# Performance work log

Hardware: AMD Instinct MI355X
Metric: run time of the kernel (lower is better)

## Reference

```python
import jax, jax.numpy as jnp
import numpy as np

N_HEADS = 16
N_EMBD = 1024

def setup_inputs() -> dict:
    key = jax.random.key(0)
    k1, k2, k3, k4, k5 = jax.random.split(key, 5)
    B, T, C = 4, 2048, N_EMBD
    x = jax.random.normal(k1, (B, T, C), dtype=jnp.float32)
    # Linear weights stored as [in, out] (equivalent math to torch's x @ W.T + b)
    W_attn = jax.random.normal(k2, (C, 3 * C), dtype=jnp.float32) * 0.02
    b_attn = jax.random.normal(k3, (3 * C,), dtype=jnp.float32) * 0.02
    W_proj = jax.random.normal(k4, (C, C), dtype=jnp.float32) * 0.02
    b_proj = jax.random.normal(k5, (C,), dtype=jnp.float32) * 0.02
    return {"x": x, "W_attn": W_attn, "b_attn": b_attn, "W_proj": W_proj, "b_proj": b_proj}

def reference(x, W_attn, b_attn, W_proj, b_proj):
    B, T, C = x.shape
    H = N_HEADS
    D = C // H
    scale = 1.0 / jnp.sqrt(jnp.asarray(D, dtype=x.dtype))
    # fused QKV projection
    qkv = x @ W_attn + b_attn                      # [B, T, 3C]
    q, k, v = jnp.split(qkv, 3, axis=-1)           # each [B, T, C]
    q = q.reshape(B, T, H, D)
    k = k.reshape(B, T, H, D)
    v = v.reshape(B, T, H, D)
    # non-causal SDPA
    scores = jnp.einsum('bqhd,bkhd->bhqk', q, k) * scale  # [B, H, T, T]
    attn = jax.nn.softmax(scores, axis=-1)
    y = jnp.einsum('bhqk,bkhd->bqhd', attn, v)     # [B, T, H, D]
    y = y.reshape(B, T, C)
    return y @ W_proj + b_proj
```

## Files before the change

### kernel.cpp

```cpp
#include <hip/hip_runtime.h>

typedef short s16x8 __attribute__((ext_vector_type(8)));
typedef short s16x4 __attribute__((ext_vector_type(4)));
typedef float f32x4 __attribute__((ext_vector_type(4)));
typedef float f32x16 __attribute__((ext_vector_type(16)));

__device__ __forceinline__ unsigned short f2bf(float f) {
  unsigned u = __float_as_uint(f);
  u += 0x7fffu + ((u >> 16) & 1u);
  return (unsigned short)(u >> 16);
}
__device__ __forceinline__ float bf2f(unsigned short h) {
  return __uint_as_float(((unsigned)h) << 16);
}

#define GLOAD_LDS16(g, l)                                          \
  __builtin_amdgcn_global_load_lds(                                \
      (const __attribute__((address_space(1))) void*)(g),          \
      (__attribute__((address_space(3))) void*)(l), 16, 0, 0)


__global__ __launch_bounds__(256) void cvt_x_bf16(const float* __restrict__ in,
                                                  unsigned short* __restrict__ out) {
  int i = (blockIdx.x * 256 + threadIdx.x) * 4;
  float4 v = *(const float4*)(in + i);
  ushort4 o;
  o.x = f2bf(v.x); o.y = f2bf(v.y); o.z = f2bf(v.z); o.w = f2bf(v.w);
  *(ushort4*)(out + i) = o;
}

__global__ __launch_bounds__(256) void transpose_w(const float* __restrict__ W,
                                                   unsigned short* __restrict__ Wt,
                                                   int R, int C) {
  __shared__ float tile[32][33];
  int c0 = blockIdx.x * 32, r0 = blockIdx.y * 32;
  int x = threadIdx.x, ty = threadIdx.y;
  for (int yy = ty; yy < 32; yy += 8)
    tile[yy][x] = W[(size_t)(r0 + yy) * C + c0 + x];
  __syncthreads();
  for (int yy = ty; yy < 32; yy += 8)
    Wt[(size_t)(c0 + yy) * R + r0 + x] = f2bf(tile[x][yy]);
}


template <int MODE>
__global__ __launch_bounds__(256) void gemm_bt(const unsigned short* __restrict__ A,
                                               const unsigned short* __restrict__ Bt,
                                               const float* __restrict__ bias,
                                               void* __restrict__ Cout,
                                               unsigned short* __restrict__ vtr,
                                               int M, int N, int K) {
  __shared__ __align__(16) unsigned short As[3][128 * 32];
  __shared__ __align__(16) unsigned short Bs[3][128 * 32];

  const int tid  = threadIdx.x;
  const int lane = tid & 63;
  const int w    = tid >> 6;
  const int lm   = lane & 31;
  const int l5   = lane >> 5;
  const int wm   = (w >> 1) * 64;
  const int wn   = (w & 1) * 64;
  const int m0   = blockIdx.x * 128;
  const int n0   = blockIdx.y * 128;

  f32x16 acc[2][2];
  for (int i = 0; i < 2; i++)
    for (int j = 0; j < 2; j++)
      for (int r = 0; r < 16; r++) acc[i][j][r] = 0.f;

  const int srow = tid >> 2;
  const int scb  = (((tid & 3) ^ ((srow >> 1) & 3)) * 8);
  const unsigned short* Ap = A  + (size_t)(m0 + srow) * K + scb;
  const unsigned short* Bp = Bt + (size_t)(n0 + srow) * K + scb;

#define STAGE_G(bb, kk)                                                  \
  do {                                                                   \
    GLOAD_LDS16(Ap + (kk), &As[bb][w * 512]);                            \
    GLOAD_LDS16(Ap + (size_t)64 * K + (kk), &As[bb][2048 + w * 512]);    \
    GLOAD_LDS16(Bp + (kk), &Bs[bb][w * 512]);                            \
    GLOAD_LDS16(Bp + (size_t)64 * K + (kk), &Bs[bb][2048 + w * 512]);    \
  } while (0)

  const int rx = ((lm >> 1) & 3) << 4;

  STAGE_G(0, 0);
  STAGE_G(1, 32);
  int cur = 0;
  for (int kk = 0; kk < K; kk += 32) {
    if (kk + 32 < K)
      asm volatile("s_waitcnt vmcnt(4)" ::: "memory");
    else
      asm volatile("s_waitcnt vmcnt(0)" ::: "memory");
    __builtin_amdgcn_s_barrier();
    __builtin_amdgcn_sched_barrier(0);

    if (kk + 64 < K) {
      int nb = cur + 2; if (nb >= 3) nb -= 3;
      STAGE_G(nb, kk + 64);
    }

    const char* Ab = (const char*)As[cur];
    const char* Bb = (const char*)Bs[cur];
    s16x8 af[2][2], bfr[2][2];
    for (int i = 0; i < 2; i++)
      for (int ks = 0; ks < 2; ks++)
        af[i][ks] = *(const s16x8*)(Ab + (wm + i * 32 + lm) * 64 +
                                    (((l5 * 16 + ks * 32)) ^ rx));
    for (int j = 0; j < 2; j++)
      for (int ks = 0; ks < 2; ks++)
        bfr[j][ks] = *(const s16x8*)(Bb + (wn + j * 32 + lm) * 64 +
                                     (((l5 * 16 + ks * 32)) ^ rx));
    for (int ks = 0; ks < 2; ks++)
      for (int i = 0; i < 2; i++)
        for (int j = 0; j < 2; j++)
          acc[i][j] = __builtin_amdgcn_mfma_f32_32x32x16_bf16(af[i][ks], bfr[j][ks],
                                                              acc[i][j], 0, 0, 0);
    cur += 1; if (cur >= 3) cur -= 3;
  }
#undef STAGE_G

  if (MODE == 1 && n0 >= 2048) {
    const int bidx = m0 >> 11;
    for (int j = 0; j < 2; j++) {
      int col = n0 + wn + j * 32 + lm;
      float bc = bias[col];
      size_t vrow = (size_t)((bidx << 10) + (col - 2048)) * 2048;
      for (int i = 0; i < 2; i++) {
        int tb = (m0 & 2047) + wm + i * 32 + l5 * 4;
        for (int g = 0; g < 4; g++) {
          ushort4 o;
          o.x = f2bf(acc[i][j][g * 4 + 0] + bc);
          o.y = f2bf(acc[i][j][g * 4 + 1] + bc);
          o.z = f2bf(acc[i][j][g * 4 + 2] + bc);
          o.w = f2bf(acc[i][j][g * 4 + 3] + bc);
          *(ushort4*)(vtr + vrow + tb + 8 * g) = o;
        }
      }
    }
  } else {
    for (int j = 0; j < 2; j++) {
      int col = n0 + wn + j * 32 + lm;
      float bc = bias[col];
      for (int i = 0; i < 2; i++) {
        int rowb = m0 + wm + i * 32 + l5 * 4;
        for (int r = 0; r < 16; r++) {
          int row = rowb + (r & 3) + 8 * (r >> 2);
          float v = acc[i][j][r] + bc;
          if (MODE == 1)
            ((unsigned short*)Cout)[(size_t)row * N + col] = f2bf(v);
          else
            ((float*)Cout)[(size_t)row * N + col] = v;
        }
      }
    }
  }
}


__global__ __launch_bounds__(256, 4) void attn_flash(const unsigned short* __restrict__ qkv,
                                                     const unsigned short* __restrict__ vt,
                                                     unsigned short* __restrict__ y) {
  const int T = 2048, C3 = 3072;
  const int bh = blockIdx.x & 63;
  const int qt = blockIdx.x >> 6;
  const int b  = bh >> 4;
  const int h  = bh & 15;
  const int q0 = qt * 128;

  const int tid  = threadIdx.x;
  const int lane = tid & 63;
  const int w    = tid >> 6;
  const int lr   = lane & 15;
  const int quad = lane >> 4;

  __shared__ __align__(16) unsigned short Ks[2][64][64];
  __shared__ __align__(16) unsigned short Vs[2][64][64];

  s16x8 qf[2][2];
  const float QSC = 0.18033688f;
  for (int j = 0; j < 2; j++)
    for (int c = 0; c < 2; c++) {
      const unsigned short* qp =
          qkv + (size_t)(b * T + q0 + w * 32 + j * 16 + lr) * C3 + h * 64 + c * 32 + quad * 8;
      s16x8 t = *(const s16x8*)qp;
      s16x8 o;
      for (int e = 0; e < 8; e++)
        o[e] = (short)f2bf(bf2f((unsigned short)t[e]) * QSC);
      qf[j][c] = o;
    }

  s16x8 ones;
  for (int e = 0; e < 8; e++) ones[e] = (short)0x3F80;

  f32x4 O[2][4];
  f32x4 Lacc[2];
  for (int j = 0; j < 2; j++) {
    for (int dt = 0; dt < 4; dt++) O[j][dt] = f32x4{0.f, 0.f, 0.f, 0.f};
    Lacc[j] = f32x4{0.f, 0.f, 0.f, 0.f};
  }

  const int srow = tid >> 3;
  const int scol = (((tid & 7) ^ (srow & 7)) * 8);
  const int kperm = (((srow & 12) << 1) | ((srow >> 4) << 2) | (srow & 3));

  const unsigned short* kbase = qkv + (size_t)(b * T) * C3 + 1024 + (size_t)h * 64;
  const unsigned short* vbase = vt + (size_t)(bh * 64) * 2048;
  const unsigned short* kp0 = kbase + (size_t)(kperm)      * C3 + scol;
  const unsigned short* kp1 = kbase + (size_t)(32 + kperm) * C3 + scol;
  const unsigned short* vp0 = vbase + (size_t)(srow)      * 2048 + scol;
  const unsigned short* vp1 = vbase + (size_t)(srow + 32) * 2048 + scol;

#define STAGE_KV(bb)                                                         \
  do {                                                                       \
    GLOAD_LDS16(kp0, &Ks[bb][w * 8][0]);                                     \
    GLOAD_LDS16(kp1, &Ks[bb][w * 8 + 32][0]);                                \
    GLOAD_LDS16(vp0, &Vs[bb][w * 8][0]);                                     \
    GLOAD_LDS16(vp1, &Vs[bb][w * 8 + 32][0]);                                \
    kp0 += (size_t)64 * C3; kp1 += (size_t)64 * C3;                          \
    vp0 += 64; vp1 += 64;                                                    \
  } while (0)

  const int rswz = (lr & 7) << 4;

#define COMPUTE(bb)                                                              \
  do {                                                                           \
    const char* KsB = (const char*)&Ks[bb][0][0];                                \
    const char* VsB = (const char*)&Vs[bb][0][0];                                \
    for (int ch = 0; ch < 2; ch++) {                                             \
      const char* krowA = KsB + (ch * 32 + lr) * 128;                            \
      const char* krowB = KsB + (ch * 32 + 16 + lr) * 128;                       \
      s16x8 kA0 = *(const s16x8*)(krowA + ((quad * 16) ^ rswz));                 \
      s16x8 kA1 = *(const s16x8*)(krowA + ((64 + quad * 16) ^ rswz));            \
      s16x8 kB0 = *(const s16x8*)(krowB + ((quad * 16) ^ rswz));                 \
      s16x8 kB1 = *(const s16x8*)(krowB + ((64 + quad * 16) ^ rswz));            \
      s16x8 vf[4];                                                               \
      for (int dt = 0; dt < 4; dt++)                                             \
        vf[dt] = *(const s16x8*)(VsB + (dt * 16 + lr) * 128 +                    \
                                 ((ch * 64 + quad * 16) ^ rswz));                \
      for (int j = 0; j < 2; j++) {                                              \
        f32x4 Sa = f32x4{0.f, 0.f, 0.f, 0.f};                                    \
        f32x4 Sb = f32x4{0.f, 0.f, 0.f, 0.f};                                    \
        __builtin_amdgcn_s_setprio(1);                                           \
        Sa = __builtin_amdgcn_mfma_f32_16x16x32_bf16(kA0, qf[j][0], Sa, 0, 0, 0);\
        Sa = __builtin_amdgcn_mfma_f32_16x16x32_bf16(kA1, qf[j][1], Sa, 0, 0, 0);\
        Sb = __builtin_amdgcn_mfma_f32_16x16x32_bf16(kB0, qf[j][0], Sb, 0, 0, 0);\
        Sb = __builtin_amdgcn_mfma_f32_16x16x32_bf16(kB1, qf[j][1], Sb, 0, 0, 0);\
        __builtin_amdgcn_s_setprio(0);                                           \
        float p0 = __builtin_amdgcn_exp2f(Sa[0]);                                \
        float p1 = __builtin_amdgcn_exp2f(Sa[1]);                                \
        float p2 = __builtin_amdgcn_exp2f(Sa[2]);                                \
        float p3 = __builtin_amdgcn_exp2f(Sa[3]);                                \
        float p4 = __builtin_amdgcn_exp2f(Sb[0]);                                \
        float p5 = __builtin_amdgcn_exp2f(Sb[1]);                                \
        float p6 = __builtin_amdgcn_exp2f(Sb[2]);                                \
        float p7 = __builtin_amdgcn_exp2f(Sb[3]);                                \
        union { unsigned u[4]; s16x8 v; } pk;                                    \
        asm("v_cvt_pk_bf16_f32 %0, %1, %2" : "=v"(pk.u[0]) : "v"(p0), "v"(p1));  \
        asm("v_cvt_pk_bf16_f32 %0, %1, %2" : "=v"(pk.u[1]) : "v"(p2), "v"(p3));  \
        asm("v_cvt_pk_bf16_f32 %0, %1, %2" : "=v"(pk.u[2]) : "v"(p4), "v"(p5));  \
        asm("v_cvt_pk_bf16_f32 %0, %1, %2" : "=v"(pk.u[3]) : "v"(p6), "v"(p7));  \
        __builtin_amdgcn_s_setprio(1);                                           \
        Lacc[j] = __builtin_amdgcn_mfma_f32_16x16x32_bf16(pk.v, ones, Lacc[j],   \
                                                          0, 0, 0);              \
        for (int dt = 0; dt < 4; dt++)                                           \
          O[j][dt] = __builtin_amdgcn_mfma_f32_16x16x32_bf16(pk.v, vf[dt],       \
                                                             O[j][dt], 0, 0, 0); \
        __builtin_amdgcn_s_setprio(0);                                           \
      }                                                                          \
    }                                                                            \
  } while (0)

  STAGE_KV(0);
  for (int kt2 = 0; kt2 < 16; kt2++) {
    __syncthreads();
    STAGE_KV(1);
    COMPUTE(0);
    __syncthreads();
    if (kt2 < 15) STAGE_KV(0);
    COMPUTE(1);
  }
#undef STAGE_KV
#undef COMPUTE

  for (int j = 0; j < 2; j++) {
    for (int r = 0; r < 4; r++) {
      float inv = 1.f / Lacc[j][r];
      int row = b * T + q0 + w * 32 + j * 16 + quad * 4 + r;
      for (int dt = 0; dt < 4; dt++) {
        int col = h * 64 + dt * 16 + lr;
        y[(size_t)row * 1024 + col] = f2bf(O[j][dt][r] * inv);
      }
    }
  }
}


extern "C" void kernel_launch(void* const* d_in, const int* in_sizes, int n_in,
                              void* d_out, int out_size, void* d_ws, size_t ws_size,
                              hipStream_t stream) {
  const float* x  = (const float*)d_in[0];
  const float* Wa = (const float*)d_in[1];
  const float* ba = (const float*)d_in[2];
  const float* Wp = (const float*)d_in[3];
  const float* bp = (const float*)d_in[4];
  float* out = (float*)d_out;

  char* ws = (char*)d_ws;
  unsigned short* xb  = (unsigned short*)ws;
  unsigned short* Wat = (unsigned short*)(ws + 16777216);
  unsigned short* Wpt = (unsigned short*)(ws + 23068672);
  unsigned short* qkv = (unsigned short*)(ws + 25165824);
  unsigned short* vtr = (unsigned short*)(ws + 75497472);

  cvt_x_bf16<<<8192, 256, 0, stream>>>(x, xb);
  transpose_w<<<dim3(96, 32), dim3(32, 8), 0, stream>>>(Wa, Wat, 1024, 3072);
  transpose_w<<<dim3(32, 32), dim3(32, 8), 0, stream>>>(Wp, Wpt, 1024, 1024);

  gemm_bt<1><<<dim3(64, 24), 256, 0, stream>>>(xb, Wat, ba, qkv, vtr, 8192, 3072, 1024);

  attn_flash<<<1024, 256, 0, stream>>>(qkv, vtr, xb);

  gemm_bt<0><<<dim3(64, 8), 256, 0, stream>>>(xb, Wpt, bp, out, nullptr, 8192, 1024, 1024);
}
```

Before: 264.9 us.

## Enlarge GEMM tiles to 256x256 with 8 waves and 4-stage split-phase pipeline

Both projection GEMMs now use 256x256 block tiles with 512 threads in a 2x4 wave grid, each wave computing 128x64 of output. The K loop moves from a 3-buffer to a 4-buffer LDS ring and splits each K-step into two halves, interleaving the A and B global-to-LDS loads with MFMA bursts under extra barriers and raised wave priority. The aim is more data reuse per LDS byte and better overlap of loads with matrix math. The cost is more LDS per block, higher register pressure, and fewer blocks (384 and 128), which may underfill the CUs, especially for the output projection.

Measured after the change: 278.5 us. 1.05x slower.

```diff
diff --git a/kernel.cpp b/kernel.cpp
--- a/kernel.cpp
+++ b/kernel.cpp
@@ -44,27 +44,27 @@
 
 
 template <int MODE>
-__global__ __launch_bounds__(256) void gemm_bt(const unsigned short* __restrict__ A,
-                                               const unsigned short* __restrict__ Bt,
-                                               const float* __restrict__ bias,
-                                               void* __restrict__ Cout,
-                                               unsigned short* __restrict__ vtr,
-                                               int M, int N, int K) {
-  __shared__ __align__(16) unsigned short As[3][128 * 32];
-  __shared__ __align__(16) unsigned short Bs[3][128 * 32];
+__global__ __launch_bounds__(512, 2) void gemm_bt(const unsigned short* __restrict__ A,
+                                                  const unsigned short* __restrict__ Bt,
+                                                  const float* __restrict__ bias,
+                                                  void* __restrict__ Cout,
+                                                  unsigned short* __restrict__ vtr,
+                                                  int M, int N, int K) {
+  __shared__ __align__(16) unsigned short As[4][256 * 32];
+  __shared__ __align__(16) unsigned short Bs[4][256 * 32];
 
   const int tid  = threadIdx.x;
   const int lane = tid & 63;
   const int w    = tid >> 6;
   const int lm   = lane & 31;
   const int l5   = lane >> 5;
-  const int wm   = (w >> 1) * 64;
-  const int wn   = (w & 1) * 64;
-  const int m0   = blockIdx.x * 128;
-  const int n0   = blockIdx.y * 128;
-
-  f32x16 acc[2][2];
-  for (int i = 0; i < 2; i++)
+  const int wr   = w >> 2;
+  const int wc   = w & 3;
+  const int m0   = blockIdx.x * 256;
+  const int n0   = blockIdx.y * 256;
+
+  f32x16 acc[4][2];
+  for (int i = 0; i < 4; i++)
     for (int j = 0; j < 2; j++)
       for (int r = 0; r < 16; r++) acc[i][j][r] = 0.f;
 
@@ -73,60 +73,82 @@
   const unsigned short* Ap = A  + (size_t)(m0 + srow) * K + scb;
   const unsigned short* Bp = Bt + (size_t)(n0 + srow) * K + scb;
 
-#define STAGE_G(bb, kk)                                                  \
-  do {                                                                   \
-    GLOAD_LDS16(Ap + (kk), &As[bb][w * 512]);                            \
-    GLOAD_LDS16(Ap + (size_t)64 * K + (kk), &As[bb][2048 + w * 512]);    \
-    GLOAD_LDS16(Bp + (kk), &Bs[bb][w * 512]);                            \
-    GLOAD_LDS16(Bp + (size_t)64 * K + (kk), &Bs[bb][2048 + w * 512]);    \
+#define STAGE_A(bb, t)                                                    \
+  do {                                                                    \
+    GLOAD_LDS16(Ap + (t) * 32, &As[bb][w * 512]);                         \
+    GLOAD_LDS16(Ap + (size_t)128 * K + (t) * 32, &As[bb][4096 + w * 512]);\
   } while (0)
+#define STAGE_B(bb, t)                                                    \
+  do {                                                                    \
+    GLOAD_LDS16(Bp + (t) * 32, &Bs[bb][w * 512]);                         \
+    GLOAD_LDS16(Bp + (size_t)128 * K + (t) * 32, &Bs[bb][4096 + w * 512]);\
+  } while (0)
 
   const int rx = ((lm >> 1) & 3) << 4;
-
-  STAGE_G(0, 0);
-  STAGE_G(1, 32);
-  int cur = 0;
-  for (int kk = 0; kk < K; kk += 32) {
-    if (kk + 32 < K)
+  const int nt = K >> 5;
+
+  STAGE_A(0, 0); STAGE_B(0, 0);
+  STAGE_A(1, 1); STAGE_B(1, 1);
+  STAGE_A(2, 2); STAGE_B(2, 2);
+
+  for (int t = 0; t < nt; t++) {
+    if (t + 2 < nt)
+      asm volatile("s_waitcnt vmcnt(8)" ::: "memory");
+    else if (t + 1 < nt)
       asm volatile("s_waitcnt vmcnt(4)" ::: "memory");
     else
       asm volatile("s_waitcnt vmcnt(0)" ::: "memory");
     __builtin_amdgcn_s_barrier();
     __builtin_amdgcn_sched_barrier(0);
 
-    if (kk + 64 < K) {
-      int nb = cur + 2; if (nb >= 3) nb -= 3;
-      STAGE_G(nb, kk + 64);
-    }
-
-    const char* Ab = (const char*)As[cur];
-    const char* Bb = (const char*)Bs[cur];
-    s16x8 af[2][2], bfr[2][2];
-    for (int i = 0; i < 2; i++)
-      for (int ks = 0; ks < 2; ks++)
-        af[i][ks] = *(const s16x8*)(Ab + (wm + i * 32 + lm) * 64 +
-                                    (((l5 * 16 + ks * 32)) ^ rx));
+    const char* Ab = (const char*)As[t & 3];
+    const char* Bb = (const char*)Bs[t & 3];
+    const int  nb = (t + 3) & 3;
+    const bool st = (t + 3) < nt;
+
+    s16x8 a0[4], b0[2];
+    for (int i = 0; i < 4; i++)
+      a0[i] = *(const s16x8*)(Ab + (wr * 128 + i * 32 + lm) * 64 + ((l5 * 16) ^ rx));
     for (int j = 0; j < 2; j++)
-      for (int ks = 0; ks < 2; ks++)
-        bfr[j][ks] = *(const s16x8*)(Bb + (wn + j * 32 + lm) * 64 +
-                                     (((l5 * 16 + ks * 32)) ^ rx));
-    for (int ks = 0; ks < 2; ks++)
-      for (int i = 0; i < 2; i++)
-        for (int j = 0; j < 2; j++)
-          acc[i][j] = __builtin_amdgcn_mfma_f32_32x32x16_bf16(af[i][ks], bfr[j][ks],
-                                                              acc[i][j], 0, 0, 0);
-    cur += 1; if (cur >= 3) cur -= 3;
-  }
-#undef STAGE_G
+      b0[j] = *(const s16x8*)(Bb + (wc * 64 + j * 32 + lm) * 64 + ((l5 * 16) ^ rx));
+    if (st) STAGE_A(nb, t + 3);
+    __builtin_amdgcn_s_barrier();
+    asm volatile("s_waitcnt lgkmcnt(0)" ::: "memory");
+    __builtin_amdgcn_sched_barrier(0);
+    __builtin_amdgcn_s_setprio(1);
+    for (int i = 0; i < 4; i++)
+      for (int j = 0; j < 2; j++)
+        acc[i][j] = __builtin_amdgcn_mfma_f32_32x32x16_bf16(a0[i], b0[j], acc[i][j], 0, 0, 0);
+    __builtin_amdgcn_s_setprio(0);
+    __builtin_amdgcn_s_barrier();
+    __builtin_amdgcn_sched_barrier(0);
+
+    s16x8 a1[4], b1[2];
+    for (int i = 0; i < 4; i++)
+      a1[i] = *(const s16x8*)(Ab + (wr * 128 + i * 32 + lm) * 64 + ((32 + l5 * 16) ^ rx));
+    for (int j = 0; j < 2; j++)
+      b1[j] = *(const s16x8*)(Bb + (wc * 64 + j * 32 + lm) * 64 + ((32 + l5 * 16) ^ rx));
+    if (st) STAGE_B(nb, t + 3);
+    __builtin_amdgcn_s_barrier();
+    asm volatile("s_waitcnt lgkmcnt(0)" ::: "memory");
+    __builtin_amdgcn_sched_barrier(0);
+    __builtin_amdgcn_s_setprio(1);
+    for (int i = 0; i < 4; i++)
+      for (int j = 0; j < 2; j++)
+        acc[i][j] = __builtin_amdgcn_mfma_f32_32x32x16_bf16(a1[i], b1[j], acc[i][j], 0, 0, 0);
+    __builtin_amdgcn_s_setprio(0);
+  }
+#undef STAGE_A
+#undef STAGE_B
 
   if (MODE == 1 && n0 >= 2048) {
     const int bidx = m0 >> 11;
     for (int j = 0; j < 2; j++) {
-      int col = n0 + wn + j * 32 + lm;
+      int col = n0 + wc * 64 + j * 32 + lm;
       float bc = bias[col];
       size_t vrow = (size_t)((bidx << 10) + (col - 2048)) * 2048;
-      for (int i = 0; i < 2; i++) {
-        int tb = (m0 & 2047) + wm + i * 32 + l5 * 4;
+      for (int i = 0; i < 4; i++) {
+        int tb = (m0 & 2047) + wr * 128 + i * 32 + l5 * 4;
         for (int g = 0; g < 4; g++) {
           ushort4 o;
           o.x = f2bf(acc[i][j][g * 4 + 0] + bc);
@@ -139,10 +161,10 @@
     }
   } else {
     for (int j = 0; j < 2; j++) {
-      int col = n0 + wn + j * 32 + lm;
+      int col = n0 + wc * 64 + j * 32 + lm;
       float bc = bias[col];
-      for (int i = 0; i < 2; i++) {
-        int rowb = m0 + wm + i * 32 + l5 * 4;
+      for (int i = 0; i < 4; i++) {
+        int rowb = m0 + wr * 128 + i * 32 + l5 * 4;
         for (int r = 0; r < 16; r++) {
           int row = rowb + (r & 3) + 8 * (r >> 2);
           float v = acc[i][j][r] + bc;
@@ -316,9 +338,9 @@
   transpose_w<<<dim3(96, 32), dim3(32, 8), 0, stream>>>(Wa, Wat, 1024, 3072);
   transpose_w<<<dim3(32, 32), dim3(32, 8), 0, stream>>>(Wp, Wpt, 1024, 1024);
 
-  gemm_bt<1><<<dim3(64, 24), 256, 0, stream>>>(xb, Wat, ba, qkv, vtr, 8192, 3072, 1024);
+  gemm_bt<1><<<dim3(32, 12), 512, 0, stream>>>(xb, Wat, ba, qkv, vtr, 8192, 3072, 1024);
 
   attn_flash<<<1024, 256, 0, stream>>>(qkv, vtr, xb);
 
-  gemm_bt<0><<<dim3(64, 8), 256, 0, stream>>>(xb, Wpt, bp, out, nullptr, 8192, 1024, 1024);
-}
+  gemm_bt<0><<<dim3(32, 4), 512, 0, stream>>>(xb, Wpt, bp, out, nullptr, 8192, 1024, 1024);
+}
```
